# Optimization experiments

Measured on AMD Instinct MI355X. Metric: run time of the kernel, lower is better.

The kernel has to match this reference:

```python
import jax, jax.numpy as jnp
import numpy as np

NBATCH, NUP, NDOWN, NMO, NCONF = 8192, 8, 8, 32, 64


def setup_inputs() -> dict:
    key = jax.random.key(0)
    k1, k2, k3, k4 = jax.random.split(key, 4)
    MO = jax.random.normal(k1, (NBATCH, NUP + NDOWN, NMO), dtype=jnp.float32)
    d2MO = jax.random.normal(k2, (NBATCH, NUP + NDOWN, NMO), dtype=jnp.float32)
    # each config = 8 distinct MO column indices per spin (distinct -> invertible A)
    configs_up = jnp.argsort(jax.random.uniform(k3, (NCONF, NMO)), axis=1)[:, :NUP].astype(jnp.int32)
    configs_down = jnp.argsort(jax.random.uniform(k4, (NCONF, NMO)), axis=1)[:, :NDOWN].astype(jnp.int32)
    return {"MO": MO, "d2MO": d2MO, "configs_up": configs_up, "configs_down": configs_down}


def _gather(M, elec_idx, cols):
    # M: (B, nelec, nmo) -> select electron rows then per-config MO columns
    Ms = M[:, elec_idx, :]                  # (B, n, nmo)
    A = jnp.take(Ms, cols, axis=2)          # (B, n, C, n)
    return jnp.transpose(A, (0, 2, 1, 3))   # (B, C, n, n)


def reference(MO, d2MO, configs_up, configs_down):
    nup = configs_up.shape[1]
    ndown = configs_down.shape[1]
    iup = jnp.arange(nup)
    idown = jnp.arange(nup, nup + ndown)

    Aup = _gather(MO, iup, configs_up)       # (B, C, nup, nup)
    Adn = _gather(MO, idown, configs_down)   # (B, C, ndown, ndown)
    d2up = _gather(d2MO, iup, configs_up)
    d2dn = _gather(d2MO, idown, configs_down)

    iAup = jnp.linalg.inv(Aup)
    iAdn = jnp.linalg.inv(Adn)

    # btrace(iA @ d2A) = sum_ij iA[i,j] * d2A[j,i]
    tr = lambda X, Y: jnp.einsum('bcij,bcji->bc', X, Y)
    out = tr(iAup, d2up) + tr(iAdn, d2dn)    # (B, C)

    # return_local_energy=False branch: multiply by product of determinants
    pd = jnp.linalg.det(Aup) * jnp.linalg.det(Adn)
    return -0.5 * out * pd
```

## Files before the change

### kernel.cpp

```cpp
#include <hip/hip_runtime.h>

#define NBATCH 8192
#define NELEC  16
#define NMO    32
#define NCONF  64
#define NS     8
#define TSTR   20
#define TSZ    (NMO * TSTR)

__device__ __forceinline__ void solve8T(const float* __restrict__ MOT,
                                        const float* __restrict__ D2T,
                                        const int (&cols)[NS], int eoff,
                                        float& det_out, float& tr_out)
{
    float A[NS][NS], D[NS][NS];
    #pragma unroll
    for (int j = 0; j < NS; ++j) {
        const float4* pa = (const float4*)(MOT + cols[j] * TSTR + eoff);
        const float4* pd = (const float4*)(D2T + cols[j] * TSTR + eoff);
        float4 a0 = pa[0], a1 = pa[1];
        float4 d0 = pd[0], d1 = pd[1];
        A[j][0] = a0.x; A[j][1] = a0.y; A[j][2] = a0.z; A[j][3] = a0.w;
        A[j][4] = a1.x; A[j][5] = a1.y; A[j][6] = a1.z; A[j][7] = a1.w;
        D[j][0] = d0.x; D[j][1] = d0.y; D[j][2] = d0.z; D[j][3] = d0.w;
        D[j][4] = d1.x; D[j][5] = d1.y; D[j][6] = d1.z; D[j][7] = d1.w;
    }

    float det = 1.0f;
    #pragma unroll
    for (int k = 0; k < NS; ++k) {
        det *= A[k][k];
        float pinv = __builtin_amdgcn_rcpf(A[k][k]);
        A[k][k] = pinv;
        #pragma unroll
        for (int r = k + 1; r < NS; ++r) {
            float m = A[r][k] * pinv;
            #pragma unroll
            for (int c2 = k + 1; c2 < NS; ++c2)
                A[r][c2] = fmaf(-m, A[k][c2], A[r][c2]);
            #pragma unroll
            for (int c2 = 0; c2 < NS; ++c2)
                D[r][c2] = fmaf(-m, D[k][c2], D[r][c2]);
        }
    }

    float tr = 0.0f;
    #pragma unroll
    for (int j = 0; j < NS; ++j) {
        float x[NS];
        #pragma unroll
        for (int i = NS - 1; i >= 0; --i) {
            if (i < j) continue;
            float acc = D[i][j];
            #pragma unroll
            for (int c2 = i + 1; c2 < NS; ++c2)
                acc = fmaf(-A[i][c2], x[c2], acc);
            x[i] = acc * A[i][i];
        }
        tr += x[j];
    }

    det_out = det;
    tr_out  = tr;
}

__global__ __launch_bounds__(256)
void KineticPooling_kernel(const float* __restrict__ MO,
                           const float* __restrict__ d2MO,
                           const int*   __restrict__ cfg_up,
                           const int*   __restrict__ cfg_dn,
                           float*       __restrict__ out)
{
    __shared__ float smem[4][2][TSZ];

    const int tid  = threadIdx.x;
    const int lane = tid & 63;
    const int wb   = tid >> 6;
    const int b    = blockIdx.x * 4 + wb;

    float* MOT = smem[wb][0];
    float* D2T = smem[wb][1];

    const float* MOb = MO   + (size_t)b * NELEC * NMO;
    const float* d2b = d2MO + (size_t)b * NELEC * NMO;

    #pragma unroll
    for (int q = 0; q < 2; ++q) {
        int r = q * 8 + (lane >> 3);
        int c = (lane & 7) * 4;
        float4 v = *(const float4*)(MOb + r * NMO + c);
        float4 w = *(const float4*)(d2b + r * NMO + c);
        MOT[(c + 0) * TSTR + r] = v.x;
        MOT[(c + 1) * TSTR + r] = v.y;
        MOT[(c + 2) * TSTR + r] = v.z;
        MOT[(c + 3) * TSTR + r] = v.w;
        D2T[(c + 0) * TSTR + r] = w.x;
        D2T[(c + 1) * TSTR + r] = w.y;
        D2T[(c + 2) * TSTR + r] = w.z;
        D2T[(c + 3) * TSTR + r] = w.w;
    }
    __syncthreads();

    int4 cu0 = ((const int4*)cfg_up)[lane * 2 + 0];
    int4 cu1 = ((const int4*)cfg_up)[lane * 2 + 1];
    int4 cd0 = ((const int4*)cfg_dn)[lane * 2 + 0];
    int4 cd1 = ((const int4*)cfg_dn)[lane * 2 + 1];
    const int cu[NS] = {cu0.x, cu0.y, cu0.z, cu0.w, cu1.x, cu1.y, cu1.z, cu1.w};
    const int cd[NS] = {cd0.x, cd0.y, cd0.z, cd0.w, cd1.x, cd1.y, cd1.z, cd1.w};

    float detU, trU, detD, trD;
    solve8T(MOT, D2T, cu, 0,  detU, trU);
    solve8T(MOT, D2T, cd, NS, detD, trD);

    out[(size_t)b * NCONF + lane] = -0.5f * (trU + trD) * detU * detD;
}

extern "C" void kernel_launch(void* const* d_in, const int* in_sizes, int n_in,
                              void* d_out, int out_size, void* d_ws, size_t ws_size,
                              hipStream_t stream)
{
    const float* MO     = (const float*)d_in[0];
    const float* d2MO   = (const float*)d_in[1];
    const int*   cfg_up = (const int*)d_in[2];
    const int*   cfg_dn = (const int*)d_in[3];
    float* out = (float*)d_out;

    dim3 grid(NBATCH / 4);
    dim3 block(256);
    KineticPooling_kernel<<<grid, block, 0, stream>>>(MO, d2MO, cfg_up, cfg_dn, out);
}
```

Baseline: 97.68 us.

## Split up/down spin solves across adjacent lanes and combine via shuffle

Each thread now handles one spin block (up or down) of one configuration instead of both, so a batch uses 128 threads and a block covers two batches instead of four. Paired lanes exchange determinant and trace with a xor shuffle, and the even lane writes the output. This doubles thread-level parallelism and halves the serial per-thread work, which should improve latency hiding. The cost is half the lanes idle at the store and the divergent choice of config pointer and electron offset.

```diff
diff --git a/kernel.cpp b/kernel.cpp
--- a/kernel.cpp
+++ b/kernel.cpp
@@ -65,29 +65,28 @@
 }
 
 __global__ __launch_bounds__(256)
-void KineticPooling_kernel(const float* __restrict__ MO,
-                           const float* __restrict__ d2MO,
-                           const int*   __restrict__ cfg_up,
-                           const int*   __restrict__ cfg_dn,
-                           float*       __restrict__ out)
+void kp_split_kernel(const float* __restrict__ MO,
+                     const float* __restrict__ d2MO,
+                     const int*   __restrict__ cfg_up,
+                     const int*   __restrict__ cfg_dn,
+                     float*       __restrict__ out)
 {
-    __shared__ float smem[4][2][TSZ];
+    __shared__ float smem[2][2][TSZ];
 
     const int tid  = threadIdx.x;
-    const int lane = tid & 63;
-    const int wb   = tid >> 6;
-    const int b    = blockIdx.x * 4 + wb;
+    const int half = tid >> 7;
+    const int u    = tid & 127;
+    const int b    = blockIdx.x * 2 + half;
 
-    float* MOT = smem[wb][0];
-    float* D2T = smem[wb][1];
+    float* MOT = smem[half][0];
+    float* D2T = smem[half][1];
 
     const float* MOb = MO   + (size_t)b * NELEC * NMO;
     const float* d2b = d2MO + (size_t)b * NELEC * NMO;
 
-    #pragma unroll
-    for (int q = 0; q < 2; ++q) {
-        int r = q * 8 + (lane >> 3);
-        int c = (lane & 7) * 4;
+    {
+        int r = u >> 3;
+        int c = (u & 7) * 4;
         float4 v = *(const float4*)(MOb + r * NMO + c);
         float4 w = *(const float4*)(d2b + r * NMO + c);
         MOT[(c + 0) * TSTR + r] = v.x;
@@ -101,18 +100,20 @@
     }
     __syncthreads();
 
-    int4 cu0 = ((const int4*)cfg_up)[lane * 2 + 0];
-    int4 cu1 = ((const int4*)cfg_up)[lane * 2 + 1];
-    int4 cd0 = ((const int4*)cfg_dn)[lane * 2 + 0];
-    int4 cd1 = ((const int4*)cfg_dn)[lane * 2 + 1];
-    const int cu[NS] = {cu0.x, cu0.y, cu0.z, cu0.w, cu1.x, cu1.y, cu1.z, cu1.w};
-    const int cd[NS] = {cd0.x, cd0.y, cd0.z, cd0.w, cd1.x, cd1.y, cd1.z, cd1.w};
+    const int cidx = u >> 1;
+    const int s    = u & 1;
+    const int* cfg = s ? cfg_dn : cfg_up;
+    int4 c0 = ((const int4*)cfg)[cidx * 2 + 0];
+    int4 c1 = ((const int4*)cfg)[cidx * 2 + 1];
+    const int cols[NS] = {c0.x, c0.y, c0.z, c0.w, c1.x, c1.y, c1.z, c1.w};
 
-    float detU, trU, detD, trD;
-    solve8T(MOT, D2T, cu, 0,  detU, trU);
-    solve8T(MOT, D2T, cd, NS, detD, trD);
+    float det, tr;
+    solve8T(MOT, D2T, cols, s * NS, det, tr);
 
-    out[(size_t)b * NCONF + lane] = -0.5f * (trU + trD) * detU * detD;
+    float det_o = __shfl_xor(det, 1);
+    float tr_o  = __shfl_xor(tr, 1);
+    if (s == 0)
+        out[(size_t)b * NCONF + cidx] = -0.5f * (tr + tr_o) * det * det_o;
 }
 
 extern "C" void kernel_launch(void* const* d_in, const int* in_sizes, int n_in,
@@ -125,7 +126,7 @@
     const int*   cfg_dn = (const int*)d_in[3];
     float* out = (float*)d_out;
 
-    dim3 grid(NBATCH / 4);
+    dim3 grid(NBATCH / 2);
     dim3 block(256);
-    KineticPooling_kernel<<<grid, block, 0, stream>>>(MO, d2MO, cfg_up, cfg_dn, out);
+    kp_split_kernel<<<grid, block, 0, stream>>>(MO, d2MO, cfg_up, cfg_dn, out);
 }
```

New measurement: 91.55 us. -6.3%, faster.
